# Kernel optimization log

Hardware: AMD Instinct MI355X
Metric: run time of the kernel (lower is better)

The kernel has to match this reference:

```python
import jax, jax.numpy as jnp
import numpy as np

F_NODE, F_BOND, D, LAYERS = 133, 14, 256, 3
N_NODE, N_BOND, N_NB = 100000, 200000, 600000


def hardswish(x):
    return x * jnp.clip(x + 3.0, 0.0, 6.0) * (1.0 / 6.0)


def setup_inputs() -> dict:
    key = jax.random.key(0)
    ks = jax.random.split(key, 16)

    def xav(k, fan_in, fan_out):
        std = (2.0 / (fan_in + fan_out)) ** 0.5
        return (jax.random.normal(k, (fan_in, fan_out), jnp.float32) * std)

    inp = {
        "node": jax.random.normal(ks[0], (N_NODE, F_NODE), jnp.float32),
        "bond": jax.random.normal(ks[1], (N_BOND, F_BOND), jnp.float32),
        "connect": jax.random.randint(ks[2], (3, N_BOND), 0, N_NODE, jnp.int32),
        "bond_neighbour": jax.random.randint(ks[3], (2, N_NB), 0, N_BOND, jnp.int32),
        # learned parameters, stored as [in, out] (torch Linear transposed)
        "w_node": xav(ks[4], F_NODE, D), "b_node": jnp.zeros((D,), jnp.float32),
        "w_node_final": xav(ks[5], F_NODE + D, D), "b_node_final": jnp.zeros((D,), jnp.float32),
        "w_bond": xav(ks[6], F_NODE + F_BOND, D), "b_bond": jnp.zeros((D,), jnp.float32),
        "w_bond_final": xav(ks[7], F_NODE + F_BOND + D, D), "b_bond_final": jnp.zeros((D,), jnp.float32),
        "w_z": xav(ks[8], F_NODE + F_BOND + D, D), "b_z": jnp.zeros((D,), jnp.float32),
        "w_r": xav(ks[9], F_NODE + F_BOND + D, D), "b_r": jnp.zeros((D,), jnp.float32),
        "u": xav(ks[10], D, D),
        "w_m": xav(ks[11], F_NODE + F_BOND, D), "b_m": jnp.zeros((D,), jnp.float32),
        "w_n": xav(ks[12], F_NODE, D), "b_n": jnp.zeros((D,), jnp.float32),
        "u_n": xav(ks[13], 2 * D, D),
    }
    return inp


def reference(node, bond, connect, bond_neighbour,
              w_node, b_node, w_node_final, b_node_final,
              w_bond, b_bond, w_bond_final, b_bond_final,
              w_z, b_z, w_r, b_r, u, w_m, b_m, w_n, b_n, u_n):
    i_idx, j_idx = connect[0], connect[1]          # [E]; connect[2] (reverse) unused
    ij_idx, ki_idx = bond_neighbour[0], bond_neighbour[1]  # [E_nb]

    init_bond = jnp.concatenate([node[i_idx], bond], axis=-1)  # [E, f_node+f_bond]
    init_node = node                                           # [N, f_node]

    mess_bond = hardswish(init_bond @ w_bond + b_bond)  # [E, D]
    mess_node = hardswish(node @ w_node + b_node)       # [N, D]

    for _ in range(LAYERS):
        mess_ki = mess_bond[ki_idx]                                   # [E_nb, D]
        s_ij = jax.ops.segment_sum(mess_ki, ij_idx, num_segments=N_BOND)
        z_ij = jax.nn.sigmoid(jnp.concatenate([init_bond, s_ij], -1) @ w_z + b_z)
        r_ki = jax.nn.sigmoid(jnp.concatenate([init_bond[ij_idx], mess_ki], -1) @ w_r + b_r)
        r_ij = jax.ops.segment_sum(r_ki * mess_ki, ij_idx, num_segments=N_BOND)
        m_ij = jnp.tanh(init_bond @ w_m + b_m + r_ij @ u)
        mess_bond = (1.0 - z_ij) * s_ij + z_ij * m_ij                 # [E, D]
        aggr_node = jax.ops.segment_sum(mess_bond, j_idx, num_segments=N_NODE)
        mess_node = hardswish(init_node @ w_n + b_n
                              + jnp.concatenate([mess_node, aggr_node], -1) @ u_n)

    mess_bond = hardswish(jnp.concatenate([init_bond, mess_bond], -1) @ w_bond_final + b_bond_final)
    mess_node = hardswish(jnp.concatenate([init_node, mess_node], -1) @ w_node_final + b_node_final)
    # dropout is identity in eval mode
    return mess_node, mess_bond
```

## Files before the change

### kernel.cpp

```cpp
#include <hip/hip_runtime.h>
#include <hip/hip_bf16.h>

#define NN 100000
#define NE 200000
#define NB 600000
#define FN 133
#define FB 14
#define FIB 147
#define DD 256
#define NEPAD (196 * 1024)
#define NNPAD (98 * 1024)

typedef __hip_bfloat16 bf16;
typedef __attribute__((ext_vector_type(8))) short short8;
typedef __attribute__((ext_vector_type(4))) float f32x4;

__device__ __forceinline__ float hswish(float x) {
    float c = fminf(fmaxf(x + 3.f, 0.f), 6.f);
    return x * c * (1.f / 6.f);
}
__device__ __forceinline__ float sigmoidf(float x) {
    return 1.f / (1.f + __expf(-x));
}
__device__ __forceinline__ float tanh_fast(float x) {
    return 1.f - 2.f / (1.f + __expf(2.f * x));
}
__device__ __forceinline__ float bf2f(unsigned short u) {
    union { unsigned int i; float f; } c; c.i = (unsigned int)u << 16; return c.f;
}
__device__ __forceinline__ unsigned short f2bf(float v) {
    bf16 b = __float2bfloat16(v);
    unsigned short u; __builtin_memcpy(&u, &b, 2); return u;
}
__device__ __forceinline__ void unp8(short8 v, float* f) {
    #pragma unroll
    for (int j = 0; j < 8; j++) {
        short s = v[j]; unsigned short u; __builtin_memcpy(&u, &s, 2);
        f[j] = bf2f(u);
    }
}
__device__ __forceinline__ uint4 pk8(const float* f) {
    uint4 v;
    v.x = f2bf(f[0]) | ((unsigned)f2bf(f[1]) << 16);
    v.y = f2bf(f[2]) | ((unsigned)f2bf(f[3]) << 16);
    v.z = f2bf(f[4]) | ((unsigned)f2bf(f[5]) << 16);
    v.w = f2bf(f[6]) | ((unsigned)f2bf(f[7]) << 16);
    return v;
}

__global__ __launch_bounds__(256) void fill_kernel(float* __restrict__ p, float v, long n4) {
    long i = (long)blockIdx.x * 256 + threadIdx.x;
    long st = (long)gridDim.x * 256;
    float4 z = {v, v, v, v};
    for (; i < n4; i += st) ((float4*)p)[i] = z;
}

__device__ __forceinline__ void ib_row(
    const float* __restrict__ node, const float* __restrict__ bond,
    const int* __restrict__ i_idx, bf16* __restrict__ IB, int row, int lane)
{
    if (lane >= 40) return;
    int src = i_idx[row];
    int c = lane * 4;
    unsigned short us[4];
    #pragma unroll
    for (int j = 0; j < 4; j++) {
        int k = c + j;
        float v = 0.f;
        if (k < FN)       v = node[(size_t)src * FN + k];
        else if (k < FIB) v = bond[(size_t)row * FB + (k - FN)];
        us[j] = f2bf(v);
    }
    ushort4 o = {us[0], us[1], us[2], us[3]};
    *(ushort4*)((unsigned short*)IB + (size_t)row * 160 + c) = o;
}

__device__ __forceinline__ void pack_body(
    int idx,
    const float* __restrict__ w_r, const float* __restrict__ w_z,
    const float* __restrict__ w_bond, const float* __restrict__ w_m,
    const float* __restrict__ w_node, const float* __restrict__ w_n,
    const float* __restrict__ u_, const float* __restrict__ u_n,
    const float* __restrict__ w_bf, const float* __restrict__ w_nf,
    bf16* __restrict__ wt)
{
    if (idx >= 786432) return;
    float v = 0.f;
    if (idx < 245760) {
        int r = idx / 40960;
        int loc = idx - r * 40960;
        int n = loc / 160, k = loc % 160;
        const float* W = (r == 0) ? w_r : (r == 1) ? w_z : (r == 2) ? w_bond
                       : (r == 3) ? w_m : (r == 4) ? w_node : w_n;
        int K1 = (r < 4) ? FIB : FN;
        if (k < K1) v = W[(size_t)k * DD + n];
    } else if (idx < 442368) {
        int r = (idx - 245760) / 65536;
        int loc = (idx - 245760) - r * 65536;
        int n = loc / 256, k = loc % 256;
        const float* W = (r == 0) ? (w_r + (size_t)FIB * DD)
                       : (r == 1) ? (w_z + (size_t)FIB * DD) : u_;
        v = W[(size_t)k * DD + n];
    } else if (idx < 573440) {
        int loc = idx - 442368;
        int n = loc / 512, k = loc % 512;
        v = u_n[(size_t)k * DD + n];
    } else {
        int r = (idx - 573440) / 106496;
        int loc = (idx - 573440) - r * 106496;
        int n = loc / 416, k = loc % 416;
        const float* W = r ? w_nf : w_bf;
        int K1 = r ? FN : FIB;
        if (k < K1)        v = W[(size_t)k * DD + n];
        else if (k >= 160) v = W[(size_t)(K1 + k - 160) * DD + n];
    }
    wt[idx] = __float2bfloat16(v);
}

__global__ __launch_bounds__(256) void zero_pack(
    int* __restrict__ offE, int* __restrict__ offN,
    const float* __restrict__ w_r, const float* __restrict__ w_z,
    const float* __restrict__ w_bond, const float* __restrict__ w_m,
    const float* __restrict__ w_node, const float* __restrict__ w_n,
    const float* __restrict__ u_, const float* __restrict__ u_n,
    const float* __restrict__ w_bf, const float* __restrict__ w_nf,
    bf16* __restrict__ wt)
{
    int b = blockIdx.x;
    if (b < 1176) {
        int i = b * 256 + threadIdx.x;
        if (i < NEPAD) offE[i] = 0;
        else if (i < NEPAD + NNPAD) offN[i - NEPAD] = 0;
    } else {
        pack_body((b - 1176) * 256 + threadIdx.x,
                  w_r, w_z, w_bond, w_m, w_node, w_n, u_, u_n, w_bf, w_nf, wt);
    }
}

__global__ __launch_bounds__(256) void count2_kernel(
    const int* __restrict__ ij, const int* __restrict__ jidx,
    int* __restrict__ offE, int* __restrict__ offN)
{
    int i = blockIdx.x * 256 + threadIdx.x;
    if (i < NB) atomicAdd(&offE[ij[i]], 1);
    else if (i < NB + NE) atomicAdd(&offN[jidx[i - NB]], 1);
}

__global__ __launch_bounds__(256) void scan_block2(
    int* __restrict__ offE, int* __restrict__ offN,
    int* __restrict__ bsumE, int* __restrict__ bsumN)
{
    __shared__ int lds[256];
    int* data; int* bs; int bb;
    if ((int)blockIdx.x < 196) { data = offE; bs = bsumE; bb = blockIdx.x; }
    else                       { data = offN; bs = bsumN; bb = blockIdx.x - 196; }
    int base = bb * 1024 + threadIdx.x * 4;
    int c0 = data[base], c1 = data[base + 1], c2 = data[base + 2], c3 = data[base + 3];
    int t = c0 + c1 + c2 + c3;
    lds[threadIdx.x] = t;
    __syncthreads();
    int x = t;
    for (int off = 1; off < 256; off <<= 1) {
        int y = (threadIdx.x >= off) ? lds[threadIdx.x - off] : 0;
        __syncthreads();
        x += y; lds[threadIdx.x] = x;
        __syncthreads();
    }
    int excl = x - t;
    data[base] = excl; data[base + 1] = excl + c0;
    data[base + 2] = excl + c0 + c1; data[base + 3] = excl + c0 + c1 + c2;
    if (threadIdx.x == 255) bs[bb] = x;
}

__global__ __launch_bounds__(256) void scan_bsum2(int* __restrict__ bsumE, int* __restrict__ bsumN)
{
    __shared__ int lds[256];
    int* bs = blockIdx.x ? bsumN : bsumE;
    int n = blockIdx.x ? 98 : 196;
    int t = (threadIdx.x < n) ? bs[threadIdx.x] : 0;
    lds[threadIdx.x] = t;
    __syncthreads();
    int x = t;
    for (int off = 1; off < 256; off <<= 1) {
        int y = (threadIdx.x >= off) ? lds[threadIdx.x - off] : 0;
        __syncthreads();
        x += y; lds[threadIdx.x] = x;
        __syncthreads();
    }
    if (threadIdx.x < n) bs[threadIdx.x] = x - t;
}

__global__ __launch_bounds__(256) void scan_add_copy2(
    int* __restrict__ offE, int* __restrict__ offN,
    const int* __restrict__ bsumE, const int* __restrict__ bsumN,
    int* __restrict__ curE, int* __restrict__ curN)
{
    int i = blockIdx.x * 256 + threadIdx.x;
    if (i < NEPAD) {
        int v = offE[i] + bsumE[i >> 10];
        offE[i] = v; curE[i] = v;
    } else if (i < NEPAD + NNPAD) {
        int j = i - NEPAD;
        int v = offN[j] + bsumN[j >> 10];
        offN[j] = v; curN[j] = v;
    }
}

__global__ __launch_bounds__(256) void lists_ib(
    const int* __restrict__ ij, const int* __restrict__ ki, const int* __restrict__ jidx,
    int* __restrict__ curE, int* __restrict__ curN,
    int* __restrict__ nbLst, int* __restrict__ agLst,
    const float* __restrict__ node, const float* __restrict__ bond,
    const int* __restrict__ i_idx, bf16* __restrict__ IB)
{
    int b = blockIdx.x;
    if (b < 3125) {
        int i = b * 256 + threadIdx.x;
        if (i < NB) { int p = atomicAdd(&curE[ij[i]], 1); nbLst[p] = ki[i]; }
        else if (i < NB + NE) {
            int e = i - NB;
            int p = atomicAdd(&curN[jidx[e]], 1); agLst[p] = e;
        }
    } else {
        int row = (b - 3125) * 4 + (threadIdx.x >> 6);
        if (row < NE) ib_row(node, bond, i_idx, IB, row, threadIdx.x & 63);
    }
}

__global__ __launch_bounds__(256) void seg_sr_kernel(
    const bf16* __restrict__ MB, const bf16* __restrict__ TR,
    const bf16* __restrict__ PR, const int* __restrict__ off,
    const int* __restrict__ lst,
    bf16* __restrict__ S, bf16* __restrict__ R)
{
    int sid = blockIdx.x * 4 + (threadIdx.x >> 6);
    if (sid >= NE) return;
    int lane = threadIdx.x & 63;
    ushort4 up = *(const ushort4*)((const unsigned short*)PR + (size_t)sid * DD + lane * 4);
    float p0 = bf2f(up.x), p1 = bf2f(up.y), p2 = bf2f(up.z), p3 = bf2f(up.w);
    int b = off[sid], e = off[sid + 1];
    float s0 = 0, s1 = 0, s2 = 0, s3 = 0;
    float r0 = 0, r1 = 0, r2 = 0, r3 = 0;
    for (int t = b; t < e; t++) {
        int src = lst[t];
        ushort4 um = *(const ushort4*)((const unsigned short*)MB + (size_t)src * DD + lane * 4);
        ushort4 ut = *(const ushort4*)((const unsigned short*)TR + (size_t)src * DD + lane * 4);
        float m0 = bf2f(um.x), m1 = bf2f(um.y), m2 = bf2f(um.z), m3 = bf2f(um.w);
        s0 += m0; s1 += m1; s2 += m2; s3 += m3;
        r0 += sigmoidf(p0 + bf2f(ut.x)) * m0;
        r1 += sigmoidf(p1 + bf2f(ut.y)) * m1;
        r2 += sigmoidf(p2 + bf2f(ut.z)) * m2;
        r3 += sigmoidf(p3 + bf2f(ut.w)) * m3;
    }
    ushort4 os = {f2bf(s0), f2bf(s1), f2bf(s2), f2bf(s3)};
    ushort4 orr = {f2bf(r0), f2bf(r1), f2bf(r2), f2bf(r3)};
    *(ushort4*)((unsigned short*)S + (size_t)sid * DD + lane * 4) = os;
    *(ushort4*)((unsigned short*)R + (size_t)sid * DD + lane * 4) = orr;
}

__global__ __launch_bounds__(512) void blend2(
    const bf16* __restrict__ S, const bf16* __restrict__ R,
    const bf16* __restrict__ WTz2, const bf16* __restrict__ WTu,
    const bf16* __restrict__ PZ, const bf16* __restrict__ PM,
    bf16* __restrict__ MB)
{
    __shared__ __align__(16) unsigned short As[128 * 72];
    __shared__ __align__(16) unsigned short Bs[128 * 72];
    const int tid = threadIdx.x;
    const int row0 = blockIdx.x * 128, col0 = blockIdx.y * 128;
    const int lane = tid & 63, w = tid >> 6;
    const int wr = w >> 1, wc = w & 1;
    const int fr = lane & 15, ko = (lane >> 4) * 8;

    f32x4 acc1[2][4] = {};
    f32x4 acc2[2][4] = {};

    #pragma unroll
    for (int ph = 0; ph < 2; ph++) {
        const bf16* A = (ph == 0) ? S : R;
        const bf16* W = (ph == 0) ? WTz2 : WTu;
        for (int k0 = 0; k0 < DD; k0 += 64) {
            {
                int mloc = tid >> 2, kq = (tid & 3) * 16;
                int mg = row0 + mloc;
                uint4 va = {0, 0, 0, 0}, va2 = {0, 0, 0, 0};
                if (mg < NE) {
                    va  = *(const uint4*)((const unsigned short*)A + (size_t)mg * DD + k0 + kq);
                    va2 = *(const uint4*)((const unsigned short*)A + (size_t)mg * DD + k0 + kq + 8);
                }
                uint4 vb  = *(const uint4*)((const unsigned short*)W + (size_t)(col0 + mloc) * DD + k0 + kq);
                uint4 vb2 = *(const uint4*)((const unsigned short*)W + (size_t)(col0 + mloc) * DD + k0 + kq + 8);
                *(uint4*)&As[mloc * 72 + kq] = va;
                *(uint4*)&As[mloc * 72 + kq + 8] = va2;
                *(uint4*)&Bs[mloc * 72 + kq] = vb;
                *(uint4*)&Bs[mloc * 72 + kq + 8] = vb2;
            }
            __syncthreads();
            #pragma unroll
            for (int kk = 0; kk < 64; kk += 32) {
                short8 af[2], bf8[4];
                #pragma unroll
                for (int mf = 0; mf < 2; mf++)
                    af[mf] = *(const short8*)&As[(wr * 32 + mf * 16 + fr) * 72 + kk + ko];
                #pragma unroll
                for (int nf = 0; nf < 4; nf++)
                    bf8[nf] = *(const short8*)&Bs[(wc * 64 + nf * 16 + fr) * 72 + kk + ko];
                #pragma unroll
                for (int mf = 0; mf < 2; mf++)
                    #pragma unroll
                    for (int nf = 0; nf < 4; nf++) {
                        if (ph == 0)
                            acc1[mf][nf] = __builtin_amdgcn_mfma_f32_16x16x32_bf16(af[mf], bf8[nf], acc1[mf][nf], 0, 0, 0);
                        else
                            acc2[mf][nf] = __builtin_amdgcn_mfma_f32_16x16x32_bf16(af[mf], bf8[nf], acc2[mf][nf], 0, 0, 0);
                    }
            }
            __syncthreads();
        }
    }

    #pragma unroll
    for (int mf = 0; mf < 2; mf++) {
        #pragma unroll
        for (int i = 0; i < 4; i++) {
            int mloc = wr * 32 + mf * 16 + (lane >> 4) * 4 + i;
            int gm = row0 + mloc;
            if (gm >= NE) continue;
            #pragma unroll
            for (int nf = 0; nf < 4; nf++) {
                int gc = col0 + wc * 64 + nf * 16 + fr;
                size_t idx = (size_t)gm * DD + gc;
                float z  = sigmoidf(acc1[mf][nf][i] + __bfloat162float(PZ[idx]));
                float mm = tanh_fast(acc2[mf][nf][i] + __bfloat162float(PM[idx]));
                float s  = __bfloat162float(S[idx]);
                MB[idx] = __float2bfloat16((1.f - z) * s + z * mm);
            }
        }
    }
}

__global__ __launch_bounds__(512) void pairk(
    int trblocks,
    const bf16* __restrict__ MBn, const bf16* __restrict__ WTr2,
    bf16* __restrict__ TRo,
    const bf16* __restrict__ MN, const int* __restrict__ offN,
    const int* __restrict__ agLst, const bf16* __restrict__ WTnu,
    const bf16* __restrict__ PN, bf16* __restrict__ MNout,
    const float* __restrict__ node, const float* __restrict__ bond,
    const int* __restrict__ i_idx, bf16* __restrict__ IBout)
{
    __shared__ __align__(16) unsigned short As[128 * 40];
    __shared__ __align__(16) unsigned short Bs[256 * 40];
    const int tid = threadIdx.x, lane = tid & 63, w = tid >> 6;
    const int fr = lane & 15, ko = (lane >> 4) * 8;
    const int mloc = tid >> 2, kq = (tid & 3) * 8;

    if ((int)blockIdx.x < trblocks) {
        const int row0 = blockIdx.x * 128;
        const int wr = w >> 2, wc = w & 3;
        const int mg = row0 + mloc;
        f32x4 acc[4][4] = {};
        for (int k0 = 0; k0 < 256; k0 += 32) {
            uint4 v = {0, 0, 0, 0};
            if (mg < NE)
                v = *(const uint4*)((const unsigned short*)MBn + (size_t)mg * DD + k0 + kq);
            *(uint4*)&As[mloc * 40 + kq] = v;
            #pragma unroll
            for (int it = 0; it < 2; ++it) {
                int nloc = (tid >> 2) + it * 128;
                *(uint4*)&Bs[nloc * 40 + kq] =
                    *(const uint4*)((const unsigned short*)WTr2 + (size_t)nloc * DD + k0 + kq);
            }
            __syncthreads();
            short8 af[4], bw[4];
            #pragma unroll
            for (int mf = 0; mf < 4; mf++)
                af[mf] = *(const short8*)&As[(wr * 64 + mf * 16 + fr) * 40 + ko];
            #pragma unroll
            for (int nf = 0; nf < 4; nf++)
                bw[nf] = *(const short8*)&Bs[(wc * 64 + nf * 16 + fr) * 40 + ko];
            #pragma unroll
            for (int mf = 0; mf < 4; mf++)
                #pragma unroll
                for (int nf = 0; nf < 4; nf++)
                    acc[mf][nf] = __builtin_amdgcn_mfma_f32_16x16x32_bf16(af[mf], bw[nf], acc[mf][nf], 0, 0, 0);
            __syncthreads();
        }
        #pragma unroll
        for (int mf = 0; mf < 4; mf++)
            #pragma unroll
            for (int i = 0; i < 4; i++) {
                int ml = wr * 64 + mf * 16 + (lane >> 4) * 4 + i;
                int gm = row0 + ml;
                if (gm >= NE) continue;
                #pragma unroll
                for (int nf = 0; nf < 4; nf++) {
                    int gc = wc * 64 + nf * 16 + fr;
                    TRo[(size_t)gm * DD + gc] = __float2bfloat16(acc[mf][nf][i]);
                }
            }
    } else if ((int)blockIdx.x < trblocks + 782) {
        const int bx = blockIdx.x - trblocks;
        const int row0 = bx * 128;
        const int wr = w >> 2, wc = w & 3;
        const int mg = row0 + mloc;
        int eb = 0, ee = 0;
        if (mg < NN) { eb = offN[mg]; ee = offN[mg + 1]; }
        f32x4 acc[4][4] = {};
        for (int k0 = 0; k0 < 512; k0 += 32) {
            const int kg = k0 + kq;
            uint4 v = {0, 0, 0, 0};
            if (mg < NN) {
                if (kg < 256) {
                    v = *(const uint4*)((const unsigned short*)MN + (size_t)mg * DD + kg);
                } else {
                    const int kk = kg - 256;
                    float a[8] = {0, 0, 0, 0, 0, 0, 0, 0};
                    for (int t = eb; t < ee; t++) {
                        int src = agLst[t];
                        float m8[8];
                        unp8(*(const short8*)((const unsigned short*)MBn + (size_t)src * DD + kk), m8);
                        #pragma unroll
                        for (int j = 0; j < 8; j++) a[j] += m8[j];
                    }
                    v = pk8(a);
                }
            }
            *(uint4*)&As[mloc * 40 + kq] = v;
            #pragma unroll
            for (int it = 0; it < 2; ++it) {
                int nloc = (tid >> 2) + it * 128;
                *(uint4*)&Bs[nloc * 40 + kq] =
                    *(const uint4*)((const unsigned short*)WTnu + (size_t)nloc * 512 + k0 + kq);
            }
            __syncthreads();
            short8 af[4], bw[4];
            #pragma unroll
            for (int mf = 0; mf < 4; mf++)
                af[mf] = *(const short8*)&As[(wr * 64 + mf * 16 + fr) * 40 + ko];
            #pragma unroll
            for (int nf = 0; nf < 4; nf++)
                bw[nf] = *(const short8*)&Bs[(wc * 64 + nf * 16 + fr) * 40 + ko];
            #pragma unroll
            for (int mf = 0; mf < 4; mf++)
                #pragma unroll
                for (int nf = 0; nf < 4; nf++)
                    acc[mf][nf] = __builtin_amdgcn_mfma_f32_16x16x32_bf16(af[mf], bw[nf], acc[mf][nf], 0, 0, 0);
            __syncthreads();
        }
        #pragma unroll
        for (int mf = 0; mf < 4; mf++)
            #pragma unroll
            for (int i = 0; i < 4; i++) {
                int ml = wr * 64 + mf * 16 + (lane >> 4) * 4 + i;
                int gm = row0 + ml;
                if (gm >= NN) continue;
                #pragma unroll
                for (int nf = 0; nf < 4; nf++) {
                    int gc = wc * 64 + nf * 16 + fr;
                    size_t idx = (size_t)gm * DD + gc;
                    MNout[idx] = __float2bfloat16(
                        hswish(acc[mf][nf][i] + __bfloat162float(PN[idx])));
                }
            }
    } else {
        int b2 = blockIdx.x - trblocks - 782;
        int row = b2 * 8 + (tid >> 6);
        if (row < NE) ib_row(node, bond, i_idx, IBout, row, lane);
    }
}

template <int BN, int NT, int DUAL, int EPB>
__device__ __forceinline__ void bg_body(
    const void* __restrict__ A1, int a1stride, int a1kw, int a1real, int a1f32,
    const void* __restrict__ A2, int a2stride, int a2kw, int a2real, int a2f32,
    const bf16* __restrict__ WT1, const bf16* __restrict__ WT2, int KT,
    const float* __restrict__ bias1, const float* __restrict__ bias2,
    void* __restrict__ out1, void* __restrict__ out2, int M,
    int row0, int col0,
    unsigned short* As, unsigned short* Bs, unsigned short* Bs2)
{
    constexpr int BM = 128;
    constexpr int nWc = BN / 64;
    constexpr int nWr = (NT / 64) / nWc;
    constexpr int MSPAN = BM / nWr;
    constexpr int MFR = MSPAN / 16;
    const int tid = threadIdx.x;
    const int lane = tid & 63, w = tid >> 6;
    const int wr = w / nWc, wc = w % nWc;
    const int fr = lane & 15, ko = (lane >> 4) * 8;

    f32x4 acc[MFR][4] = {};
    f32x4 acc2[DUAL ? MFR : 1][DUAL ? 4 : 1] = {};

    for (int k0 = 0; k0 < KT; k0 += 32) {
        #pragma unroll
        for (int it = 0; it < BM * 4 / NT; ++it) {
            int mloc = (tid >> 2) + it * (NT / 4);
            int mg = row0 + mloc;
            bool mok = (mg < M);
            int kq = (tid & 3) * 8;
            int kg = k0 + kq;
            const void* p; int stride, real, isf; int kk;
            if (kg < a1kw) { p = A1; stride = a1stride; real = a1real; isf = a1f32; kk = kg; }
            else           { p = A2; stride = a2stride; real = a2real; isf = a2f32; kk = kg - a1kw; }
            uint4 v = {0, 0, 0, 0};
            if (mok) {
                if (!isf) {
                    v = *(const uint4*)((const bf16*)p + (size_t)mg * stride + kk);
                } else {
                    const float* fp = (const float*)p + (size_t)mg * stride;
                    unsigned short us[8];
                    #pragma unroll
                    for (int j = 0; j < 8; j++)
                        us[j] = (kk + j < real) ? f2bf(fp[kk + j]) : (unsigned short)0;
                    v.x = us[0] | ((unsigned)us[1] << 16);
                    v.y = us[2] | ((unsigned)us[3] << 16);
                    v.z = us[4] | ((unsigned)us[5] << 16);
                    v.w = us[6] | ((unsigned)us[7] << 16);
                }
            }
            *(uint4*)&As[mloc * 40 + kq] = v;
        }
        #pragma unroll
        for (int it = 0; it < BN * 4 / NT; ++it) {
            int nloc = (tid >> 2) + it * (NT / 4);
            int kq = (tid & 3) * 8;
            *(uint4*)&Bs[nloc * 40 + kq] =
                *(const uint4*)&WT1[(size_t)(col0 + nloc) * KT + k0 + kq];
            if (DUAL)
                *(uint4*)&Bs2[nloc * 40 + kq] =
                    *(const uint4*)&WT2[(size_t)(col0 + nloc) * KT + k0 + kq];
        }
        __syncthreads();
        short8 a1f[MFR], b1f[4], b2f[DUAL ? 4 : 1];
        #pragma unroll
        for (int mf = 0; mf < MFR; mf++)
            a1f[mf] = *(const short8*)&As[(wr * MSPAN + mf * 16 + fr) * 40 + ko];
        #pragma unroll
        for (int nf = 0; nf < 4; nf++) {
            b1f[nf] = *(const short8*)&Bs[(wc * 64 + nf * 16 + fr) * 40 + ko];
            if (DUAL)
                b2f[nf] = *(const short8*)&Bs2[(wc * 64 + nf * 16 + fr) * 40 + ko];
        }
        #pragma unroll
        for (int mf = 0; mf < MFR; mf++)
            #pragma unroll
            for (int nf = 0; nf < 4; nf++) {
                acc[mf][nf] = __builtin_amdgcn_mfma_f32_16x16x32_bf16(a1f[mf], b1f[nf], acc[mf][nf], 0, 0, 0);
                if (DUAL)
                    acc2[mf][nf] = __builtin_amdgcn_mfma_f32_16x16x32_bf16(a1f[mf], b2f[nf], acc2[mf][nf], 0, 0, 0);
            }
        __syncthreads();
    }

    #pragma unroll
    for (int mf = 0; mf < MFR; mf++) {
        #pragma unroll
        for (int i = 0; i < 4; i++) {
            int mloc = wr * MSPAN + mf * 16 + (lane >> 4) * 4 + i;
            int gm = row0 + mloc;
            if (gm >= M) continue;
            #pragma unroll
            for (int nf = 0; nf < 4; nf++) {
                int gc = col0 + wc * 64 + nf * 16 + fr;
                size_t idx = (size_t)gm * DD + gc;
                float v = acc[mf][nf][i];
                if (EPB == 0) {
                    if (bias1) v += bias1[gc];
                    ((bf16*)out1)[idx] = __float2bfloat16(v);
                } else if (EPB == 2) {
                    ((bf16*)out1)[idx] = __float2bfloat16(hswish(v + bias1[gc]));
                    ((bf16*)out2)[idx] = __float2bfloat16(acc2[mf][nf][i] + bias2[gc]);
                } else if (EPB == 3) {
                    ((bf16*)out1)[idx] = __float2bfloat16(v + bias1[gc]);
                    ((bf16*)out2)[idx] = __float2bfloat16(acc2[mf][nf][i] + bias2[gc]);
                } else {
                    ((float*)out1)[idx] = hswish(v + bias1[gc]);
                }
            }
        }
    }
}

__device__ __forceinline__ void bg64_body(
    const void* __restrict__ A1, int a1stride, int a1kw, int a1real, int a1f32,
    const void* __restrict__ A2, int a2stride, int a2kw, int a2real, int a2f32,
    const bf16* __restrict__ WT1, int KT, const float* __restrict__ bias1,
    float* __restrict__ out1, int M, int row0,
    unsigned short* As, unsigned short* Bs)
{
    const int tid = threadIdx.x;
    const int lane = tid & 63, w = tid >> 6;
    const int wr = w >> 2, wc = w & 3;
    const int fr = lane & 15, ko = (lane >> 4) * 8;

    f32x4 acc[2][4] = {};

    for (int k0 = 0; k0 < KT; k0 += 32) {
        if (tid < 256) {
            int mloc = tid >> 2, kq = (tid & 3) * 8;
            int mg = row0 + mloc;
            int kg = k0 + kq;
            const void* p; int stride, real, isf; int kk;
            if (kg < a1kw) { p = A1; stride = a1stride; real = a1real; isf = a1f32; kk = kg; }
            else           { p = A2; stride = a2stride; real = a2real; isf = a2f32; kk = kg - a1kw; }
            uint4 v = {0, 0, 0, 0};
            if (mg < M) {
                if (!isf) {
                    v = *(const uint4*)((const bf16*)p + (size_t)mg * stride + kk);
                } else {
                    const float* fp = (const float*)p + (size_t)mg * stride;
                    unsigned short us[8];
                    #pragma unroll
                    for (int j = 0; j < 8; j++)
                        us[j] = (kk + j < real) ? f2bf(fp[kk + j]) : (unsigned short)0;
                    v.x = us[0] | ((unsigned)us[1] << 16);
                    v.y = us[2] | ((unsigned)us[3] << 16);
                    v.z = us[4] | ((unsigned)us[5] << 16);
                    v.w = us[6] | ((unsigned)us[7] << 16);
                }
            }
            *(uint4*)&As[mloc * 40 + kq] = v;
        }
        {
            int kq = (tid & 3) * 8;
            #pragma unroll
            for (int it = 0; it < 2; ++it) {
                int nloc = (tid >> 2) + it * 128;
                *(uint4*)&Bs[nloc * 40 + kq] =
                    *(const uint4*)&WT1[(size_t)nloc * KT + k0 + kq];
            }
        }
        __syncthreads();
        short8 af[2], bw[4];
        #pragma unroll
        for (int mf = 0; mf < 2; mf++)
            af[mf] = *(const short8*)&As[(wr * 32 + mf * 16 + fr) * 40 + ko];
        #pragma unroll
        for (int nf = 0; nf < 4; nf++)
            bw[nf] = *(const short8*)&Bs[(wc * 64 + nf * 16 + fr) * 40 + ko];
        #pragma unroll
        for (int mf = 0; mf < 2; mf++)
            #pragma unroll
            for (int nf = 0; nf < 4; nf++)
                acc[mf][nf] = __builtin_amdgcn_mfma_f32_16x16x32_bf16(af[mf], bw[nf], acc[mf][nf], 0, 0, 0);
        __syncthreads();
    }

    #pragma unroll
    for (int mf = 0; mf < 2; mf++) {
        #pragma unroll
        for (int i = 0; i < 4; i++) {
            int mloc = wr * 32 + mf * 16 + (lane >> 4) * 4 + i;
            int gm = row0 + mloc;
            if (gm >= M) continue;
            #pragma unroll
            for (int nf = 0; nf < 4; nf++) {
                int gc = wc * 64 + nf * 16 + fr;
                out1[(size_t)gm * DD + gc] = hswish(acc[mf][nf][i] + bias1[gc]);
            }
        }
    }
}

__global__ __launch_bounds__(512) void pre_pair1(
    const bf16* __restrict__ IBbf,
    const bf16* __restrict__ WTr, const bf16* __restrict__ WTz1,
    const float* __restrict__ b_r, const float* __restrict__ b_z,
    bf16* __restrict__ PR, bf16* __restrict__ PZ,
    const bf16* __restrict__ WTb, const bf16* __restrict__ WTm1,
    const float* __restrict__ b_bond, const float* __restrict__ b_m,
    bf16* __restrict__ MB, bf16* __restrict__ PM)
{
    __shared__ __align__(16) unsigned short As[128 * 40];
    __shared__ __align__(16) unsigned short Bs[128 * 40];
    __shared__ __align__(16) unsigned short Bs2[128 * 40];
    int b = blockIdx.x;
    if (b < 3126) {
        int bx = b % 1563, by = b / 1563;
        bg_body<128, 512, 1, 3>(IBbf, 160, 160, 160, 0, nullptr, 0, 0, 0, 0,
            WTr, WTz1, 160, b_r, b_z, PR, PZ, NE, bx * 128, by * 128, As, Bs, Bs2);
    } else {
        int b2 = b - 3126;
        int bx = b2 % 1563, by = b2 / 1563;
        bg_body<128, 512, 1, 2>(IBbf, 160, 160, 160, 0, nullptr, 0, 0, 0, 0,
            WTb, WTm1, 160, b_bond, b_m, MB, PM, NE, bx * 128, by * 128, As, Bs, Bs2);
    }
}

__global__ __launch_bounds__(512) void pre_pair2(
    const float* __restrict__ node,
    const bf16* __restrict__ WTn0, const bf16* __restrict__ WTn,
    const float* __restrict__ b_node, const float* __restrict__ b_n,
    bf16* __restrict__ MN, bf16* __restrict__ PN,
    const bf16* __restrict__ MB, const bf16* __restrict__ WTr2,
    bf16* __restrict__ TR)
{
    __shared__ __align__(16) unsigned short As[128 * 40];
    __shared__ __align__(16) unsigned short Bs[128 * 40];
    __shared__ __align__(16) unsigned short Bs2[128 * 40];
    int b = blockIdx.x;
    if (b < 1564) {
        int bx = b % 782, by = b / 782;
        bg_body<128, 512, 1, 2>(node, FN, 160, FN, 1, nullptr, 0, 0, 0, 0,
            WTn0, WTn, 160, b_node, b_n, MN, PN, NN, bx * 128, by * 128, As, Bs, Bs2);
    } else {
        int b2 = b - 1564;
        int bx = b2 % 1563, by = b2 / 1563;
        bg_body<128, 512, 0, 0>(MB, 256, 256, 256, 0, nullptr, 0, 0, 0, 0,
            WTr2, nullptr, 256, nullptr, nullptr, TR, nullptr, NE,
            bx * 128, by * 128, As, Bs, Bs2);
    }
}

__global__ __launch_bounds__(512) void final_pair64(
    const bf16* __restrict__ IBbf, const bf16* __restrict__ MB,
    const bf16* __restrict__ WTbf, const float* __restrict__ b_bf,
    float* __restrict__ out_bond,
    const float* __restrict__ node, const bf16* __restrict__ MNf,
    const bf16* __restrict__ WTnf, const float* __restrict__ b_nf,
    float* __restrict__ out_node)
{
    __shared__ __align__(16) unsigned short As[64 * 40];
    __shared__ __align__(16) unsigned short Bs[256 * 40];
    int b = blockIdx.x;
    if (b < 3125) {
        bg64_body(IBbf, 160, 160, 160, 0, MB, 256, 256, 256, 0,
                  WTbf, 416, b_bf, out_bond, NE, b * 64, As, Bs);
    } else {
        bg64_body(node, FN, 160, FN, 1, MNf, 256, 256, 256, 0,
                  WTnf, 416, b_nf, out_node, NN, (b - 3125) * 64, As, Bs);
    }
}

extern "C" void kernel_launch(void* const* d_in, const int* in_sizes, int n_in,
                              void* d_out, int out_size, void* d_ws, size_t ws_size,
                              hipStream_t stream)
{
    const float* node  = (const float*)d_in[0];
    const float* bond  = (const float*)d_in[1];
    const int* connect = (const int*)d_in[2];
    const int* bnb     = (const int*)d_in[3];
    const float* w_node       = (const float*)d_in[4];
    const float* b_node       = (const float*)d_in[5];
    const float* w_node_final = (const float*)d_in[6];
    const float* b_node_final = (const float*)d_in[7];
    const float* w_bond       = (const float*)d_in[8];
    const float* b_bond       = (const float*)d_in[9];
    const float* w_bond_final = (const float*)d_in[10];
    const float* b_bond_final = (const float*)d_in[11];
    const float* w_z = (const float*)d_in[12];
    const float* b_z = (const float*)d_in[13];
    const float* w_r = (const float*)d_in[14];
    const float* b_r = (const float*)d_in[15];
    const float* u_  = (const float*)d_in[16];
    const float* w_m = (const float*)d_in[17];
    const float* b_m = (const float*)d_in[18];
    const float* w_n = (const float*)d_in[19];
    const float* b_n = (const float*)d_in[20];
    const float* u_n = (const float*)d_in[21];

    const int* i_idx = connect;
    const int* j_idx = connect + NE;
    const int* ij    = bnb;
    const int* ki    = bnb + NB;

    const size_t EBH = (size_t)NE * DD * 2;
    const size_t B_WT = (size_t)786432 * 2;
    const size_t B_CSR = (size_t)NEPAD * 8 + (size_t)NB * 4
                       + (size_t)NNPAD * 8 + (size_t)NE * 4 + 2048;
    const size_t NEED = 5 * EBH + B_WT + B_CSR;

    float* out_node = (float*)d_out;
    float* out_bond = out_node + (size_t)NN * DD;

    if (ws_size < NEED) {
        fill_kernel<<<2048, 256, 0, stream>>>((float*)d_out, 1e6f, (long)out_size / 4);
        return;
    }

    char* base = (char*)d_ws;
    bf16* PR = (bf16*)base;                       base += EBH;
    bf16* MB = (bf16*)base;                       base += EBH;
    bf16* TR = (bf16*)base;                       base += EBH;
    bf16* PZ = (bf16*)base;                       base += EBH;
    bf16* PM = (bf16*)base;                       base += EBH;
    char* wt = base;                              base += B_WT;
    int* offE  = (int*)base;                      base += (size_t)NEPAD * 4;
    int* curE  = (int*)base;                      base += (size_t)NEPAD * 4;
    int* nbLst = (int*)base;                      base += (size_t)NB * 4;
    int* offN  = (int*)base;                      base += (size_t)NNPAD * 4;
    int* curN  = (int*)base;                      base += (size_t)NNPAD * 4;
    int* agLst = (int*)base;                      base += (size_t)NE * 4;
    int* bsumE = (int*)base;                      base += 1024;
    int* bsumN = (int*)base;

    bf16* IBbf = TR;
    bf16* MNf = PR;
    bf16* R = (bf16*)out_bond;
    bf16* S = R + (size_t)NE * DD;
    bf16* MN = (bf16*)out_node;
    bf16* PN = MN + (size_t)NN * DD;

    bf16* wtb = (bf16*)wt;
    bf16* WTr  = wtb + 0;
    bf16* WTz1 = wtb + 40960;
    bf16* WTb  = wtb + 81920;
    bf16* WTm1 = wtb + 122880;
    bf16* WTn0 = wtb + 163840;
    bf16* WTn  = wtb + 204800;
    bf16* WTr2 = wtb + 245760;
    bf16* WTz2 = wtb + 311296;
    bf16* WTu  = wtb + 376832;
    bf16* WTnu = wtb + 442368;
    bf16* WTbf = wtb + 573440;
    bf16* WTnf = wtb + 679936;

    zero_pack<<<1176 + 3072, 256, 0, stream>>>(offE, offN,
        w_r, w_z, w_bond, w_m, w_node, w_n, u_, u_n,
        w_bond_final, w_node_final, wtb);
    count2_kernel<<<3125, 256, 0, stream>>>(ij, j_idx, offE, offN);
    scan_block2<<<294, 256, 0, stream>>>(offE, offN, bsumE, bsumN);
    scan_bsum2<<<2, 256, 0, stream>>>(bsumE, bsumN);
    scan_add_copy2<<<1176, 256, 0, stream>>>(offE, offN, bsumE, bsumN, curE, curN);
    lists_ib<<<3125 + 50000, 256, 0, stream>>>(ij, ki, j_idx, curE, curN,
                                               nbLst, agLst, node, bond, i_idx, IBbf);

    dim3 gB2(1563, 2);

    pre_pair1<<<6252, 512, 0, stream>>>(IBbf, WTr, WTz1, b_r, b_z, PR, PZ,
                                        WTb, WTm1, b_bond, b_m, MB, PM);
    pre_pair2<<<4690, 512, 0, stream>>>(node, WTn0, WTn, b_node, b_n, MN, PN,
                                        MB, WTr2, TR);

    for (int l = 0; l < 3; l++) {
        seg_sr_kernel<<<(NE + 3) / 4, 256, 0, stream>>>(MB, TR, PR, offE, nbLst, S, R);
        blend2<<<gB2, 512, 0, stream>>>(S, R, WTz2, WTu, PZ, PM, MB);
        int trb = (l < 2) ? 1563 : 0;
        int ibb = (l == 2) ? 25000 : 0;
        bf16* mnout = (l == 2) ? MNf : MN;
        pairk<<<trb + 782 + ibb, 512, 0, stream>>>(trb, MB, WTr2, TR,
                                                   MN, offN, agLst, WTnu, PN, mnout,
                                                   node, bond, i_idx, IBbf);
    }

    final_pair64<<<4688, 512, 0, stream>>>(IBbf, MB, WTbf, b_bond_final, out_bond,
                                           node, MNf, WTnf, b_node_final, out_node);
}
```

Measured before the change: 2.399 ms.

## Merge bond precompute GEMMs sharing A tile; use full-width tile for TR

Replaces the two pre-pass kernels with one kernel. The 128x160 bond A tile is loaded into LDS once and reused for both dual-GEMM phases (r/z, then bond/m), which halves the global reads of the init_bond rows. The initial TR = MB·WTr2 product moves to its own kernel with a 128x256 output tile, so A is read once per row block instead of twice. The cost is larger LDS use (about 42KB for the A tile), which may lower occupancy, plus one extra launch.

```diff
diff --git a/kernel.cpp b/kernel.cpp
--- a/kernel.cpp
+++ b/kernel.cpp
@@ -470,117 +470,217 @@
     }
 }
 
-template <int BN, int NT, int DUAL, int EPB>
-__device__ __forceinline__ void bg_body(
-    const void* __restrict__ A1, int a1stride, int a1kw, int a1real, int a1f32,
-    const void* __restrict__ A2, int a2stride, int a2kw, int a2real, int a2f32,
-    const bf16* __restrict__ WT1, const bf16* __restrict__ WT2, int KT,
-    const float* __restrict__ bias1, const float* __restrict__ bias2,
-    void* __restrict__ out1, void* __restrict__ out2, int M,
-    int row0, int col0,
-    unsigned short* As, unsigned short* Bs, unsigned short* Bs2)
-{
-    constexpr int BM = 128;
-    constexpr int nWc = BN / 64;
-    constexpr int nWr = (NT / 64) / nWc;
-    constexpr int MSPAN = BM / nWr;
-    constexpr int MFR = MSPAN / 16;
+__global__ __launch_bounds__(512) void pre_quad(
+    const bf16* __restrict__ IBbf,
+    const bf16* __restrict__ WTr, const bf16* __restrict__ WTz1,
+    const float* __restrict__ b_r, const float* __restrict__ b_z,
+    bf16* __restrict__ PR, bf16* __restrict__ PZ,
+    const bf16* __restrict__ WTb, const bf16* __restrict__ WTm1,
+    const float* __restrict__ b_bond, const float* __restrict__ b_m,
+    bf16* __restrict__ MB, bf16* __restrict__ PM,
+    const float* __restrict__ node,
+    const bf16* __restrict__ WTn0, const bf16* __restrict__ WTn,
+    const float* __restrict__ b_node, const float* __restrict__ b_n,
+    bf16* __restrict__ MN, bf16* __restrict__ PN)
+{
+    __shared__ __align__(16) unsigned short Af[128 * 168];
+    __shared__ __align__(16) unsigned short B1[128 * 40];
+    __shared__ __align__(16) unsigned short B2[128 * 40];
     const int tid = threadIdx.x;
     const int lane = tid & 63, w = tid >> 6;
-    const int wr = w / nWc, wc = w % nWc;
     const int fr = lane & 15, ko = (lane >> 4) * 8;
-
-    f32x4 acc[MFR][4] = {};
-    f32x4 acc2[DUAL ? MFR : 1][DUAL ? 4 : 1] = {};
-
-    for (int k0 = 0; k0 < KT; k0 += 32) {
-        #pragma unroll
-        for (int it = 0; it < BM * 4 / NT; ++it) {
-            int mloc = (tid >> 2) + it * (NT / 4);
+    int b = blockIdx.x;
+
+    if (b < 3126) {
+        const int bx = b % 1563, by = b / 1563;
+        const int row0 = bx * 128, col0 = by * 128;
+        const int wr = w >> 1, wc = w & 1;
+        #pragma unroll
+        for (int it = 0; it < 5; ++it) {
+            int idx = tid + it * 512;
+            int mloc = idx / 20, kq = (idx % 20) * 8;
             int mg = row0 + mloc;
-            bool mok = (mg < M);
-            int kq = (tid & 3) * 8;
-            int kg = k0 + kq;
-            const void* p; int stride, real, isf; int kk;
-            if (kg < a1kw) { p = A1; stride = a1stride; real = a1real; isf = a1f32; kk = kg; }
-            else           { p = A2; stride = a2stride; real = a2real; isf = a2f32; kk = kg - a1kw; }
             uint4 v = {0, 0, 0, 0};
-            if (mok) {
-                if (!isf) {
-                    v = *(const uint4*)((const bf16*)p + (size_t)mg * stride + kk);
-                } else {
-                    const float* fp = (const float*)p + (size_t)mg * stride;
+            if (mg < NE)
+                v = *(const uint4*)((const unsigned short*)IBbf + (size_t)mg * 160 + kq);
+            *(uint4*)&Af[mloc * 168 + kq] = v;
+        }
+        __syncthreads();
+
+        #pragma unroll
+        for (int ph = 0; ph < 2; ph++) {
+            const bf16* W1 = ph ? WTb : WTr;
+            const bf16* W2 = ph ? WTm1 : WTz1;
+            f32x4 a1[2][4] = {};
+            f32x4 a2[2][4] = {};
+            for (int k0 = 0; k0 < 160; k0 += 32) {
+                {
+                    int nloc = tid >> 2, kq = (tid & 3) * 8;
+                    *(uint4*)&B1[nloc * 40 + kq] =
+                        *(const uint4*)((const unsigned short*)W1 + (size_t)(col0 + nloc) * 160 + k0 + kq);
+                    *(uint4*)&B2[nloc * 40 + kq] =
+                        *(const uint4*)((const unsigned short*)W2 + (size_t)(col0 + nloc) * 160 + k0 + kq);
+                }
+                __syncthreads();
+                short8 af[2], b1f[4], b2f[4];
+                #pragma unroll
+                for (int mf = 0; mf < 2; mf++)
+                    af[mf] = *(const short8*)&Af[(wr * 32 + mf * 16 + fr) * 168 + k0 + ko];
+                #pragma unroll
+                for (int nf = 0; nf < 4; nf++) {
+                    b1f[nf] = *(const short8*)&B1[(wc * 64 + nf * 16 + fr) * 40 + ko];
+                    b2f[nf] = *(const short8*)&B2[(wc * 64 + nf * 16 + fr) * 40 + ko];
+                }
+                #pragma unroll
+                for (int mf = 0; mf < 2; mf++)
+                    #pragma unroll
+                    for (int nf = 0; nf < 4; nf++) {
+                        a1[mf][nf] = __builtin_amdgcn_mfma_f32_16x16x32_bf16(af[mf], b1f[nf], a1[mf][nf], 0, 0, 0);
+                        a2[mf][nf] = __builtin_amdgcn_mfma_f32_16x16x32_bf16(af[mf], b2f[nf], a2[mf][nf], 0, 0, 0);
+                    }
+                __syncthreads();
+            }
+            #pragma unroll
+            for (int mf = 0; mf < 2; mf++)
+                #pragma unroll
+                for (int i = 0; i < 4; i++) {
+                    int mloc = wr * 32 + mf * 16 + (lane >> 4) * 4 + i;
+                    int gm = row0 + mloc;
+                    if (gm >= NE) continue;
+                    #pragma unroll
+                    for (int nf = 0; nf < 4; nf++) {
+                        int gc = col0 + wc * 64 + nf * 16 + fr;
+                        size_t idx = (size_t)gm * DD + gc;
+                        if (ph == 0) {
+                            PR[idx] = __float2bfloat16(a1[mf][nf][i] + b_r[gc]);
+                            PZ[idx] = __float2bfloat16(a2[mf][nf][i] + b_z[gc]);
+                        } else {
+                            MB[idx] = __float2bfloat16(hswish(a1[mf][nf][i] + b_bond[gc]));
+                            PM[idx] = __float2bfloat16(a2[mf][nf][i] + b_m[gc]);
+                        }
+                    }
+                }
+        }
+    } else {
+        const int b2 = b - 3126;
+        const int bx = b2 % 782, by = b2 / 782;
+        const int row0 = bx * 128, col0 = by * 128;
+        const int wr = w >> 1, wc = w & 1;
+        f32x4 a1[2][4] = {};
+        f32x4 a2[2][4] = {};
+        for (int k0 = 0; k0 < 160; k0 += 32) {
+            {
+                int mloc = tid >> 2, kq = (tid & 3) * 8;
+                int mg = row0 + mloc;
+                uint4 v = {0, 0, 0, 0};
+                if (mg < NN) {
+                    const float* fp = node + (size_t)mg * FN;
                     unsigned short us[8];
                     #pragma unroll
-                    for (int j = 0; j < 8; j++)
-                        us[j] = (kk + j < real) ? f2bf(fp[kk + j]) : (unsigned short)0;
+                    for (int j = 0; j < 8; j++) {
+                        int kk = k0 + kq + j;
+                        us[j] = (kk < FN) ? f2bf(fp[kk]) : (unsigned short)0;
+                    }
                     v.x = us[0] | ((unsigned)us[1] << 16);
                     v.y = us[2] | ((unsigned)us[3] << 16);
                     v.z = us[4] | ((unsigned)us[5] << 16);
                     v.w = us[6] | ((unsigned)us[7] << 16);
                 }
-            }
-            *(uint4*)&As[mloc * 40 + kq] = v;
-        }
-        #pragma unroll
-        for (int it = 0; it < BN * 4 / NT; ++it) {
-            int nloc = (tid >> 2) + it * (NT / 4);
-            int kq = (tid & 3) * 8;
+                *(uint4*)&Af[mloc * 40 + kq] = v;
+                *(uint4*)&B1[mloc * 40 + kq] =
+                    *(const uint4*)((const unsigned short*)WTn0 + (size_t)(col0 + mloc) * 160 + k0 + kq);
+                *(uint4*)&B2[mloc * 40 + kq] =
+                    *(const uint4*)((const unsigned short*)WTn + (size_t)(col0 + mloc) * 160 + k0 + kq);
+            }
+            __syncthreads();
+            short8 af[2], b1f[4], b2f[4];
+            #pragma unroll
+            for (int mf = 0; mf < 2; mf++)
+                af[mf] = *(const short8*)&Af[(wr * 32 + mf * 16 + fr) * 40 + ko];
+            #pragma unroll
+            for (int nf = 0; nf < 4; nf++) {
+                b1f[nf] = *(const short8*)&B1[(wc * 64 + nf * 16 + fr) * 40 + ko];
+                b2f[nf] = *(const short8*)&B2[(wc * 64 + nf * 16 + fr) * 40 + ko];
+            }
+            #pragma unroll
+            for (int mf = 0; mf < 2; mf++)
+                #pragma unroll
+                for (int nf = 0; nf < 4; nf++) {
+                    a1[mf][nf] = __builtin_amdgcn_mfma_f32_16x16x32_bf16(af[mf], b1f[nf], a1[mf][nf], 0, 0, 0);
+                    a2[mf][nf] = __builtin_amdgcn_mfma_f32_16x16x32_bf16(af[mf], b2f[nf], a2[mf][nf], 0, 0, 0);
+                }
+            __syncthreads();
+        }
+        #pragma unroll
+        for (int mf = 0; mf < 2; mf++)
+            #pragma unroll
+            for (int i = 0; i < 4; i++) {
+                int mloc = wr * 32 + mf * 16 + (lane >> 4) * 4 + i;
+                int gm = row0 + mloc;
+                if (gm >= NN) continue;
+                #pragma unroll
+                for (int nf = 0; nf < 4; nf++) {
+                    int gc = col0 + wc * 64 + nf * 16 + fr;
+                    size_t idx = (size_t)gm * DD + gc;
+                    MN[idx] = __float2bfloat16(hswish(a1[mf][nf][i] + b_node[gc]));
+                    PN[idx] = __float2bfloat16(a2[mf][nf][i] + b_n[gc]);
+                }
+            }
+    }
+}
+
+__global__ __launch_bounds__(512) void tr0_kernel(
+    const bf16* __restrict__ MBn, const bf16* __restrict__ WTr2,
+    bf16* __restrict__ TRo)
+{
+    __shared__ __align__(16) unsigned short As[128 * 40];
+    __shared__ __align__(16) unsigned short Bs[256 * 40];
+    const int tid = threadIdx.x, lane = tid & 63, w = tid >> 6;
+    const int fr = lane & 15, ko = (lane >> 4) * 8;
+    const int mloc = tid >> 2, kq = (tid & 3) * 8;
+    const int row0 = blockIdx.x * 128;
+    const int wr = w >> 2, wc = w & 3;
+    const int mg = row0 + mloc;
+    f32x4 acc[4][4] = {};
+    for (int k0 = 0; k0 < 256; k0 += 32) {
+        uint4 v = {0, 0, 0, 0};
+        if (mg < NE)
+            v = *(const uint4*)((const unsigned short*)MBn + (size_t)mg * DD + k0 + kq);
+        *(uint4*)&As[mloc * 40 + kq] = v;
+        #pragma unroll
+        for (int it = 0; it < 2; ++it) {
+            int nloc = (tid >> 2) + it * 128;
             *(uint4*)&Bs[nloc * 40 + kq] =
-                *(const uint4*)&WT1[(size_t)(col0 + nloc) * KT + k0 + kq];
-            if (DUAL)
-                *(uint4*)&Bs2[nloc * 40 + kq] =
-                    *(const uint4*)&WT2[(size_t)(col0 + nloc) * KT + k0 + kq];
+                *(const uint4*)((const unsigned short*)WTr2 + (size_t)nloc * DD + k0 + kq);
         }
         __syncthreads();
-        short8 a1f[MFR], b1f[4], b2f[DUAL ? 4 : 1];
-        #pragma unroll
-        for (int mf = 0; mf < MFR; mf++)
-            a1f[mf] = *(const short8*)&As[(wr * MSPAN + mf * 16 + fr) * 40 + ko];
-        #pragma unroll
-        for (int nf = 0; nf < 4; nf++) {
-            b1f[nf] = *(const short8*)&Bs[(wc * 64 + nf * 16 + fr) * 40 + ko];
-            if (DUAL)
-                b2f[nf] = *(const short8*)&Bs2[(wc * 64 + nf * 16 + fr) * 40 + ko];
-        }
-        #pragma unroll
-        for (int mf = 0; mf < MFR; mf++)
+        short8 af[4], bw[4];
+        #pragma unroll
+        for (int mf = 0; mf < 4; mf++)
+            af[mf] = *(const short8*)&As[(wr * 64 + mf * 16 + fr) * 40 + ko];
+        #pragma unroll
+        for (int nf = 0; nf < 4; nf++)
+            bw[nf] = *(const short8*)&Bs[(wc * 64 + nf * 16 + fr) * 40 + ko];
+        #pragma unroll
+        for (int mf = 0; mf < 4; mf++)
+            #pragma unroll
+            for (int nf = 0; nf < 4; nf++)
+                acc[mf][nf] = __builtin_amdgcn_mfma_f32_16x16x32_bf16(af[mf], bw[nf], acc[mf][nf], 0, 0, 0);
+        __syncthreads();
+    }
+    #pragma unroll
+    for (int mf = 0; mf < 4; mf++)
+        #pragma unroll
+        for (int i = 0; i < 4; i++) {
+            int ml = wr * 64 + mf * 16 + (lane >> 4) * 4 + i;
+            int gm = row0 + ml;
+            if (gm >= NE) continue;
             #pragma unroll
             for (int nf = 0; nf < 4; nf++) {
-                acc[mf][nf] = __builtin_amdgcn_mfma_f32_16x16x32_bf16(a1f[mf], b1f[nf], acc[mf][nf], 0, 0, 0);
-                if (DUAL)
-                    acc2[mf][nf] = __builtin_amdgcn_mfma_f32_16x16x32_bf16(a1f[mf], b2f[nf], acc2[mf][nf], 0, 0, 0);
-            }
-        __syncthreads();
-    }
-
-    #pragma unroll
-    for (int mf = 0; mf < MFR; mf++) {
-        #pragma unroll
-        for (int i = 0; i < 4; i++) {
-            int mloc = wr * MSPAN + mf * 16 + (lane >> 4) * 4 + i;
-            int gm = row0 + mloc;
-            if (gm >= M) continue;
-            #pragma unroll
-            for (int nf = 0; nf < 4; nf++) {
-                int gc = col0 + wc * 64 + nf * 16 + fr;
-                size_t idx = (size_t)gm * DD + gc;
-                float v = acc[mf][nf][i];
-                if (EPB == 0) {
-                    if (bias1) v += bias1[gc];
-                    ((bf16*)out1)[idx] = __float2bfloat16(v);
-                } else if (EPB == 2) {
-                    ((bf16*)out1)[idx] = __float2bfloat16(hswish(v + bias1[gc]));
-                    ((bf16*)out2)[idx] = __float2bfloat16(acc2[mf][nf][i] + bias2[gc]);
-                } else if (EPB == 3) {
-                    ((bf16*)out1)[idx] = __float2bfloat16(v + bias1[gc]);
-                    ((bf16*)out2)[idx] = __float2bfloat16(acc2[mf][nf][i] + bias2[gc]);
-                } else {
-                    ((float*)out1)[idx] = hswish(v + bias1[gc]);
-                }
-            }
-        }
-    }
+                int gc = wc * 64 + nf * 16 + fr;
+                TRo[(size_t)gm * DD + gc] = __float2bfloat16(acc[mf][nf][i]);
+            }
+        }
 }
 
 __device__ __forceinline__ void bg64_body(
@@ -664,56 +764,6 @@
     }
 }
 
-__global__ __launch_bounds__(512) void pre_pair1(
-    const bf16* __restrict__ IBbf,
-    const bf16* __restrict__ WTr, const bf16* __restrict__ WTz1,
-    const float* __restrict__ b_r, const float* __restrict__ b_z,
-    bf16* __restrict__ PR, bf16* __restrict__ PZ,
-    const bf16* __restrict__ WTb, const bf16* __restrict__ WTm1,
-    const float* __restrict__ b_bond, const float* __restrict__ b_m,
-    bf16* __restrict__ MB, bf16* __restrict__ PM)
-{
-    __shared__ __align__(16) unsigned short As[128 * 40];
-    __shared__ __align__(16) unsigned short Bs[128 * 40];
-    __shared__ __align__(16) unsigned short Bs2[128 * 40];
-    int b = blockIdx.x;
-    if (b < 3126) {
-        int bx = b % 1563, by = b / 1563;
-        bg_body<128, 512, 1, 3>(IBbf, 160, 160, 160, 0, nullptr, 0, 0, 0, 0,
-            WTr, WTz1, 160, b_r, b_z, PR, PZ, NE, bx * 128, by * 128, As, Bs, Bs2);
-    } else {
-        int b2 = b - 3126;
-        int bx = b2 % 1563, by = b2 / 1563;
-        bg_body<128, 512, 1, 2>(IBbf, 160, 160, 160, 0, nullptr, 0, 0, 0, 0,
-            WTb, WTm1, 160, b_bond, b_m, MB, PM, NE, bx * 128, by * 128, As, Bs, Bs2);
-    }
-}
-
-__global__ __launch_bounds__(512) void pre_pair2(
-    const float* __restrict__ node,
-    const bf16* __restrict__ WTn0, const bf16* __restrict__ WTn,
-    const float* __restrict__ b_node, const float* __restrict__ b_n,
-    bf16* __restrict__ MN, bf16* __restrict__ PN,
-    const bf16* __restrict__ MB, const bf16* __restrict__ WTr2,
-    bf16* __restrict__ TR)
-{
-    __shared__ __align__(16) unsigned short As[128 * 40];
-    __shared__ __align__(16) unsigned short Bs[128 * 40];
-    __shared__ __align__(16) unsigned short Bs2[128 * 40];
-    int b = blockIdx.x;
-    if (b < 1564) {
-        int bx = b % 782, by = b / 782;
-        bg_body<128, 512, 1, 2>(node, FN, 160, FN, 1, nullptr, 0, 0, 0, 0,
-            WTn0, WTn, 160, b_node, b_n, MN, PN, NN, bx * 128, by * 128, As, Bs, Bs2);
-    } else {
-        int b2 = b - 1564;
-        int bx = b2 % 1563, by = b2 / 1563;
-        bg_body<128, 512, 0, 0>(MB, 256, 256, 256, 0, nullptr, 0, 0, 0, 0,
-            WTr2, nullptr, 256, nullptr, nullptr, TR, nullptr, NE,
-            bx * 128, by * 128, As, Bs, Bs2);
-    }
-}
-
 __global__ __launch_bounds__(512) void final_pair64(
     const bf16* __restrict__ IBbf, const bf16* __restrict__ MB,
     const bf16* __restrict__ WTbf, const float* __restrict__ b_bf,
@@ -829,10 +879,11 @@
 
     dim3 gB2(1563, 2);
 
-    pre_pair1<<<6252, 512, 0, stream>>>(IBbf, WTr, WTz1, b_r, b_z, PR, PZ,
-                                        WTb, WTm1, b_bond, b_m, MB, PM);
-    pre_pair2<<<4690, 512, 0, stream>>>(node, WTn0, WTn, b_node, b_n, MN, PN,
-                                        MB, WTr2, TR);
+    pre_quad<<<4690, 512, 0, stream>>>(IBbf,
+        WTr, WTz1, b_r, b_z, PR, PZ,
+        WTb, WTm1, b_bond, b_m, MB, PM,
+        node, WTn0, WTn, b_node, b_n, MN, PN);
+    tr0_kernel<<<1563, 512, 0, stream>>>(MB, WTr2, TR);
 
     for (int l = 0; l < 3; l++) {
         seg_sr_kernel<<<(NE + 3) / 4, 256, 0, stream>>>(MB, TR, PR, offE, nbLst, S, R);
```

Result: no change. 2.395 ms (-0.2%).
